# Optimization experiments

Measured on AMD Instinct MI355X. Metric: run time of the kernel, lower is better.

Reference implementation:

```python
import jax, jax.numpy as jnp
import numpy as np

EPS = 1e-5
S = 192  # seq_len = 24*8
D = 512
DFF = 2048


def setup_inputs() -> dict:
    key = jax.random.key(0)
    ks = jax.random.split(key, 8)
    tgt = jax.random.normal(ks[0], (64, 24, 8, D), jnp.float32)
    memory = jax.random.normal(ks[1], (64, 24, 8, D), jnp.float32)
    W1 = jax.random.normal(ks[2], (D, D), jnp.float32) * 0.02
    b1 = jnp.zeros((D,), jnp.float32)
    se = jax.random.normal(ks[3], (S, S), jnp.float32)
    score_embed = (se + se.T).reshape(1, 1, S, S)
    W2 = jax.random.normal(ks[4], (DFF, S), jnp.float32) * 0.05
    b2 = jnp.zeros((DFF,), jnp.float32)
    W3 = jax.random.normal(ks[5], (1, DFF), jnp.float32) * 0.02
    b3 = jnp.zeros((1,), jnp.float32)
    return {
        'tgt': tgt, 'memory': memory,
        'W1': W1, 'b1': b1, 'score_embed': score_embed,
        'g1': jnp.ones((1,), jnp.float32), 'be1': jnp.zeros((1,), jnp.float32),
        'W2': W2, 'b2': b2,
        'g2': jnp.ones((DFF,), jnp.float32), 'be2': jnp.zeros((DFF,), jnp.float32),
        'W3': W3, 'b3': b3,
        'g3': jnp.ones((1,), jnp.float32), 'be3': jnp.zeros((1,), jnp.float32),
    }


def _bn(x, gamma, beta, axes):
    # BatchNorm in training mode: biased variance over `axes`.
    mean = jnp.mean(x, axis=axes, keepdims=True)
    var = jnp.mean((x - mean) ** 2, axis=axes, keepdims=True)
    return gamma * (x - mean) * jax.lax.rsqrt(var + EPS) + beta


def reference(tgt, memory, W1, b1, score_embed, g1, be1, W2, b2, g2, be2, W3, b3, g3, be3):
    q = tgt.shape[0]
    k = memory.shape[0]
    d = tgt.shape[-1]
    tgt = tgt.reshape(q, S, d)      # [q, t, d]
    memory = memory.reshape(k, S, d)  # [k, s, d]
    query = tgt @ W1.T + b1
    key = memory @ W1.T + b1
    # bilinear score with learned symmetric bias: [q, k, s, t]
    score = jnp.einsum('qtd,ksd->qkst', query, key) * jax.nn.sigmoid(score_embed)
    score = score.reshape(q * k, S, S)
    # dual-axis max pooling, concat -> [q*k, 2S]
    score = jnp.concatenate((score.max(axis=1), score.max(axis=2)), axis=-1)
    x = score.reshape(-1, 1, S)                       # [2qk, 1, S]
    x = _bn(x, g1.reshape(1, 1, 1), be1.reshape(1, 1, 1), (0, 2)).reshape(-1, S)
    x = x @ W2.T + b2                                 # [2qk, DFF]
    x = _bn(x, g2, be2, (0,))
    x = jax.nn.relu(x)
    x = x @ W3.T + b3                                 # [2qk, 1]
    x = x.reshape(-1, 2).sum(axis=-1, keepdims=True)  # [qk, 1]
    x = _bn(x, g3, be3, (0,))
    return x.reshape(q, k)
```

## Files before the change

### kernel.cpp

```cpp
#include <hip/hip_runtime.h>

#define SS 192
#define DD 512
#define DFF 2048
#define NROW 12288
#define EPSV 1e-5f

using bf16x8 = __attribute__((ext_vector_type(8))) __bf16;
using f32x4  = __attribute__((ext_vector_type(4))) float;

__device__ inline unsigned short f2bf(float f) {
    unsigned u = __float_as_uint(f);
    unsigned r = (u + 0x7FFFu + ((u >> 16) & 1u)) >> 16;
    return (unsigned short)r;
}
__device__ inline float bf2f(unsigned short h) {
    return __uint_as_float(((unsigned)h) << 16);
}
__device__ inline unsigned f2mono(float f) {
    unsigned u = __float_as_uint(f);
    return u ^ ((unsigned)((int)u >> 31) | 0x80000000u);
}
__device__ inline float mono2f(unsigned u) {
    unsigned b = (u & 0x80000000u) ? (u ^ 0x80000000u) : ~u;
    return __uint_as_float(b);
}
#define ENC_NEGINF 0x007FFFFFu

#define GLL16(g, l) __builtin_amdgcn_global_load_lds( \
    (const __attribute__((address_space(1))) void*)(g), \
    (__attribute__((address_space(3))) void*)(l), 16, 0, 0)

template<int NW>
__device__ inline float blockReduceSum(float v) {
    __shared__ float red[NW];
    #pragma unroll
    for (int o = 32; o > 0; o >>= 1) v += __shfl_down(v, o);
    int w = threadIdx.x >> 6;
    __syncthreads();
    if ((threadIdx.x & 63) == 0) red[w] = v;
    __syncthreads();
    if (threadIdx.x == 0) {
        float t = 0;
        #pragma unroll
        for (int i = 0; i < NW; i++) t += red[i];
        red[0] = t;
    }
    __syncthreads();
    return red[0];
}

__global__ void k_cvt(const float* __restrict__ src, unsigned short* __restrict__ dst) {
    int i = blockIdx.x * 256 + threadIdx.x;
    float4 v = ((const float4*)src)[i];
    unsigned short o[4] = { f2bf(v.x), f2bf(v.y), f2bf(v.z), f2bf(v.w) };
    ((uint2*)dst)[i] = *(uint2*)o;
}

__global__ void k_sig(const float* __restrict__ se, float* __restrict__ sig) {
    int i = blockIdx.x * 256 + threadIdx.x;
    sig[i] = 1.0f / (1.0f + __expf(-se[i]));
}

__global__ void k_rowsum(const float* __restrict__ W2, float* __restrict__ rowsum) {
    int f = blockIdx.x * 256 + threadIdx.x;
    float s = 0.f;
    for (int i = 0; i < SS; i++) s += W2[(size_t)f * SS + i];
    rowsum[f] = s;
}

__global__ __launch_bounds__(256) void k_proj(
    const unsigned short* __restrict__ xbf, const unsigned short* __restrict__ w1bf,
    const float* __restrict__ b1, unsigned short* __restrict__ outQK)
{
    __shared__ unsigned short sA[3][128 * 32];
    __shared__ unsigned short sB[3][128 * 32];
    const int tid = threadIdx.x;
    const int lane = tid & 63;
    const int w = tid >> 6;
    const int m0 = blockIdx.x * 128;
    const int n0 = blockIdx.y * 128;
    const int wm = (w >> 1) * 64, wn = (w & 1) * 64;

    f32x4 acc[4][4] = {};

    const int sr  = lane >> 2;
    const int scg = (lane & 3) ^ ((lane >> 3) & 3);
    const unsigned short* Ab = xbf  + (size_t)m0 * DD;
    const unsigned short* Bb = w1bf + (size_t)n0 * DD;
    const unsigned short* AsrcB = Ab + (size_t)(w * 2 * 16 + sr) * DD + scg * 8;
    const unsigned short* BsrcB = Bb + (size_t)(w * 2 * 16 + sr) * DD + scg * 8;

    const int l16 = lane & 15, g = lane >> 4;
    const int cswz = ((g ^ ((l16 >> 1) & 3))) * 8;

    #pragma unroll
    for (int pt = 0; pt < 2; pt++) {
        #pragma unroll
        for (int i = 0; i < 2; i++) {
            int rb = w * 2 + i;
            GLL16(AsrcB + (size_t)i * 16 * DD + pt * 32, &sA[pt][rb * 512]);
            GLL16(BsrcB + (size_t)i * 16 * DD + pt * 32, &sB[pt][rb * 512]);
        }
    }

    #pragma unroll
    for (int t = 0; t < 16; t++) {
        if (t < 15) asm volatile("s_waitcnt vmcnt(4)" ::: "memory");
        else        asm volatile("s_waitcnt vmcnt(0)" ::: "memory");
        __builtin_amdgcn_s_barrier();
        if (t + 2 < 16) {
            const int buf = (t + 2) % 3;
            const int k0  = (t + 2) * 32;
            #pragma unroll
            for (int i = 0; i < 2; i++) {
                int rb = w * 2 + i;
                GLL16(AsrcB + (size_t)i * 16 * DD + k0, &sA[buf][rb * 512]);
                GLL16(BsrcB + (size_t)i * 16 * DD + k0, &sB[buf][rb * 512]);
            }
        }
        const int cur = t % 3;
        const unsigned short* aBase = &sA[cur][(wm + l16) * 32 + cswz];
        const unsigned short* bBase = &sB[cur][(wn + l16) * 32 + cswz];
        bf16x8 af[4];
        #pragma unroll
        for (int mi = 0; mi < 4; mi++) af[mi] = *(const bf16x8*)(aBase + mi * 512);
        __builtin_amdgcn_s_setprio(1);
        #pragma unroll
        for (int ni = 0; ni < 4; ni++) {
            bf16x8 bfr = *(const bf16x8*)(bBase + ni * 512);
            #pragma unroll
            for (int mi = 0; mi < 4; mi++)
                acc[mi][ni] = __builtin_amdgcn_mfma_f32_16x16x32_bf16(af[mi], bfr, acc[mi][ni], 0, 0, 0);
        }
        __builtin_amdgcn_s_setprio(0);
    }

    const int rg = lane >> 4;
    #pragma unroll
    for (int ni = 0; ni < 4; ni++) {
        int e = n0 + wn + ni * 16 + l16;
        float bias = b1[e];
        #pragma unroll
        for (int mi = 0; mi < 4; mi++) {
            #pragma unroll
            for (int r = 0; r < 4; r++) {
                int row = m0 + wm + mi * 16 + rg * 4 + r;
                outQK[(size_t)row * DD + e] = f2bf(acc[mi][ni][r] + bias);
            }
        }
    }
}

__global__ __launch_bounds__(1024, 4) void k_score(
    const unsigned short* __restrict__ qB,
    const unsigned short* __restrict__ kB,
    const float* __restrict__ sig,
    float* __restrict__ pooled)
{
    __shared__ unsigned short sA[3][192 * 32];
    __shared__ unsigned short sB[3][192 * 32];
    __shared__ unsigned maxT[192];
    __shared__ unsigned maxS[192];

    const int tid = threadIdx.x;
    const int p = blockIdx.x;
    const int q = p >> 6, kk = p & 63;
    const unsigned short* Ab = kB + (size_t)kk * SS * DD;
    const unsigned short* Bb = qB + (size_t)q * SS * DD;

    if (tid < 192) { maxT[tid] = ENC_NEGINF; maxS[tid] = ENC_NEGINF; }

    const int lane = tid & 63, w = tid >> 6;
    const int wsr = (w >> 2) * 48;
    const int wtc = (w & 3) * 48;

    f32x4 acc[3][3] = {};

    const int sr  = lane >> 2;
    const int scg = (lane & 3) ^ ((lane >> 3) & 3);
    const bool stager = (w < 12);
    const bool isA = (w < 6);
    const int wg = (isA ? w : (w - 6)) * 2;
    const unsigned short* srcB = (isA ? Ab : Bb) + (size_t)(wg * 16 + sr) * DD + scg * 8;
    unsigned short* dst0 = isA ? &sA[0][0] : &sB[0][0];

    const int l16 = lane & 15, g = lane >> 4;
    const int cswz = ((g ^ ((l16 >> 1) & 3))) * 8;

    if (stager) {
        #pragma unroll
        for (int pt = 0; pt < 2; pt++) {
            #pragma unroll
            for (int i = 0; i < 2; i++)
                GLL16(srcB + (size_t)i * 16 * DD + pt * 32, dst0 + pt * (192 * 32) + (wg + i) * 512);
        }
    }

    #pragma unroll
    for (int t = 0; t < 16; t++) {
        if (t < 15) asm volatile("s_waitcnt vmcnt(2)" ::: "memory");
        else        asm volatile("s_waitcnt vmcnt(0)" ::: "memory");
        __builtin_amdgcn_s_barrier();
        if (t + 2 < 16 && stager) {
            const int buf = (t + 2) % 3;
            const int k0  = (t + 2) * 32;
            #pragma unroll
            for (int i = 0; i < 2; i++)
                GLL16(srcB + (size_t)i * 16 * DD + k0, dst0 + buf * (192 * 32) + (wg + i) * 512);
        }
        const int cur = t % 3;
        const unsigned short* aBase = &sA[cur][(wsr + l16) * 32 + cswz];
        const unsigned short* bBase = &sB[cur][(wtc + l16) * 32 + cswz];
        bf16x8 af[3];
        #pragma unroll
        for (int mi = 0; mi < 3; mi++) af[mi] = *(const bf16x8*)(aBase + mi * 512);
        __builtin_amdgcn_s_setprio(1);
        #pragma unroll
        for (int ni = 0; ni < 3; ni++) {
            bf16x8 bfr = *(const bf16x8*)(bBase + ni * 512);
            #pragma unroll
            for (int mi = 0; mi < 3; mi++)
                acc[mi][ni] = __builtin_amdgcn_mfma_f32_16x16x32_bf16(af[mi], bfr, acc[mi][ni], 0, 0, 0);
        }
        __builtin_amdgcn_s_setprio(0);
    }

    const int rg = lane >> 4;

    #pragma unroll
    for (int mi = 0; mi < 3; mi++) {
        #pragma unroll
        for (int r = 0; r < 4; r++) {
            int s = wsr + mi * 16 + rg * 4 + r;
            const float* srow = sig + (size_t)s * SS + wtc;
            #pragma unroll
            for (int ni = 0; ni < 3; ni++)
                acc[mi][ni][r] *= srow[ni * 16 + l16];
        }
    }

    #pragma unroll
    for (int ni = 0; ni < 3; ni++) {
        float cm = -INFINITY;
        #pragma unroll
        for (int mi = 0; mi < 3; mi++)
            #pragma unroll
            for (int r = 0; r < 4; r++)
                cm = fmaxf(cm, acc[mi][ni][r]);
        cm = fmaxf(cm, __shfl_xor(cm, 16));
        cm = fmaxf(cm, __shfl_xor(cm, 32));
        if (lane < 16) atomicMax(&maxT[wtc + ni * 16 + lane], f2mono(cm));
    }
    #pragma unroll
    for (int mi = 0; mi < 3; mi++) {
        #pragma unroll
        for (int r = 0; r < 4; r++) {
            float rm = -INFINITY;
            #pragma unroll
            for (int ni = 0; ni < 3; ni++) rm = fmaxf(rm, acc[mi][ni][r]);
            rm = fmaxf(rm, __shfl_xor(rm, 1));
            rm = fmaxf(rm, __shfl_xor(rm, 2));
            rm = fmaxf(rm, __shfl_xor(rm, 4));
            rm = fmaxf(rm, __shfl_xor(rm, 8));
            if ((lane & 15) == 0)
                atomicMax(&maxS[wsr + mi * 16 + rg * 4 + r], f2mono(rm));
        }
    }
    __syncthreads();
    float* out = pooled + (size_t)p * 384;
    if (tid < 192) {
        out[tid]       = mono2f(maxT[tid]);
        out[192 + tid] = mono2f(maxS[tid]);
    }
}

__global__ __launch_bounds__(256) void k_bn1(const float* __restrict__ pooled, float* __restrict__ bn1) {
    float s = 0.f, ss = 0.f;
    size_t base = (size_t)blockIdx.x * 8192;
    for (int i = 0; i < 32; i++) {
        float v = pooled[base + i * 256 + threadIdx.x];
        s += v; ss += v * v;
    }
    s  = blockReduceSum<4>(s);
    ss = blockReduceSum<4>(ss);
    if (threadIdx.x == 0) { atomicAdd(&bn1[0], s); atomicAdd(&bn1[1], ss); }
}

__global__ __launch_bounds__(256) void k_w2(
    const float* __restrict__ x, const float* __restrict__ W2,
    const float* __restrict__ b2, const float* __restrict__ rowsum,
    const float* __restrict__ bn1, const float* __restrict__ g1,
    const float* __restrict__ be1, unsigned short* __restrict__ z,
    float* __restrict__ cs, float* __restrict__ css)
{
    __shared__ unsigned short lA[128][40];
    __shared__ unsigned short lB[128][40];
    const int tid = threadIdx.x;
    const int lane = tid & 63;
    const int w = tid >> 6;
    const int m0 = blockIdx.x * 128;
    const int n0 = blockIdx.y * 128;
    const int wm = (w >> 1) * 64, wn = (w & 1) * 64;

    f32x4 acc[4][4] = {};
    const int srow = tid >> 1;
    const int scol = (tid & 1) * 16;
    const float* Asrc = x  + (size_t)(m0 + srow) * SS;
    const float* Bsrc = W2 + (size_t)(n0 + srow) * SS;

    for (int k0 = 0; k0 < SS; k0 += 32) {
        {
            unsigned short tmp[16];
            const float4* s4 = (const float4*)(Asrc + k0 + scol);
            #pragma unroll
            for (int i = 0; i < 4; i++) {
                float4 v = s4[i];
                tmp[i*4+0] = f2bf(v.x); tmp[i*4+1] = f2bf(v.y);
                tmp[i*4+2] = f2bf(v.z); tmp[i*4+3] = f2bf(v.w);
            }
            *(uint4*)(&lA[srow][scol])     = *(uint4*)(&tmp[0]);
            *(uint4*)(&lA[srow][scol + 8]) = *(uint4*)(&tmp[8]);
            const float4* t4 = (const float4*)(Bsrc + k0 + scol);
            #pragma unroll
            for (int i = 0; i < 4; i++) {
                float4 v = t4[i];
                tmp[i*4+0] = f2bf(v.x); tmp[i*4+1] = f2bf(v.y);
                tmp[i*4+2] = f2bf(v.z); tmp[i*4+3] = f2bf(v.w);
            }
            *(uint4*)(&lB[srow][scol])     = *(uint4*)(&tmp[0]);
            *(uint4*)(&lB[srow][scol + 8]) = *(uint4*)(&tmp[8]);
        }
        __syncthreads();
        const int l16 = lane & 15, kg = (lane >> 4) * 8;
        bf16x8 af[4];
        #pragma unroll
        for (int mi = 0; mi < 4; mi++)
            af[mi] = *(const bf16x8*)(&lA[wm + mi*16 + l16][kg]);
        #pragma unroll
        for (int ni = 0; ni < 4; ni++) {
            bf16x8 bfr = *(const bf16x8*)(&lB[wn + ni*16 + l16][kg]);
            #pragma unroll
            for (int mi = 0; mi < 4; mi++)
                acc[mi][ni] = __builtin_amdgcn_mfma_f32_16x16x32_bf16(af[mi], bfr, acc[mi][ni], 0, 0, 0);
        }
        __syncthreads();
    }

    const float n1 = 8192.0f * 192.0f;
    const float m1 = bn1[0] / n1;
    const float v1 = bn1[1] / n1 - m1 * m1;
    const float a1 = g1[0] * rsqrtf(v1 + EPSV);
    const float c1 = be1[0] - m1 * a1;

    float* colsum = (float*)&lA[0][0];
    float* colssq = colsum + 128;
    if (tid < 128) { colsum[tid] = 0.f; colssq[tid] = 0.f; }
    __syncthreads();

    const int l16 = lane & 15, rg = lane >> 4;
    #pragma unroll
    for (int ni = 0; ni < 4; ni++) {
        int lc = wn + ni*16 + l16;
        int f = n0 + lc;
        float add = c1 * rowsum[f] + b2[f];
        float s_ = 0.f, ss_ = 0.f;
        #pragma unroll
        for (int mi = 0; mi < 4; mi++) {
            #pragma unroll
            for (int r = 0; r < 4; r++) {
                int row = m0 + wm + mi*16 + rg*4 + r;
                float y = a1 * acc[mi][ni][r] + add;
                z[(size_t)row * DFF + f] = f2bf(y);
                s_ += y; ss_ += y * y;
            }
        }
        atomicAdd(&colsum[lc], s_);
        atomicAdd(&colssq[lc], ss_);
    }
    __syncthreads();
    if (tid < 128) {
        atomicAdd(&cs[n0 + tid],  colsum[tid]);
        atomicAdd(&css[n0 + tid], colssq[tid]);
    }
}

__global__ __launch_bounds__(256) void k_final_dot(
    const unsigned short* __restrict__ z, const float* __restrict__ cs,
    const float* __restrict__ css, const float* __restrict__ g2,
    const float* __restrict__ be2, const float* __restrict__ W3,
    const float* __restrict__ b3, float* __restrict__ rowout)
{
    const int lane = threadIdx.x & 63, w = threadIdx.x >> 6;
    float4 av[4][2], cv[4][2], wv[4][2];
    #pragma unroll
    for (int c = 0; c < 4; c++) {
        int col = c * 512 + lane * 8;
        #pragma unroll
        for (int h = 0; h < 2; h++) {
            float4 csv  = *(const float4*)(cs  + col + 4*h);
            float4 cssv = *(const float4*)(css + col + 4*h);
            float4 g2v  = *(const float4*)(g2  + col + 4*h);
            float4 be2v = *(const float4*)(be2 + col + 4*h);
            wv[c][h]    = *(const float4*)(W3  + col + 4*h);
            float* mp = (float*)&csv; float* sp = (float*)&cssv;
            float* gp = (float*)&g2v; float* bp = (float*)&be2v;
            float* ap = (float*)&av[c][h]; float* cp = (float*)&cv[c][h];
            #pragma unroll
            for (int j = 0; j < 4; j++) {
                float m  = mp[j] * (1.0f / 8192.0f);
                float vr = sp[j] * (1.0f / 8192.0f) - m * m;
                float a  = gp[j] * rsqrtf(vr + EPSV);
                ap[j] = a;
                cp[j] = bp[j] - m * a;
            }
        }
    }
    const float bias = b3[0];
    int r0 = blockIdx.x * 16 + w * 4;
    #pragma unroll
    for (int rr = 0; rr < 4; rr++) {
        int row = r0 + rr;
        float sum = 0.f;
        #pragma unroll
        for (int c = 0; c < 4; c++) {
            uint4 v = *(const uint4*)(z + (size_t)row * DFF + c * 512 + lane * 8);
            unsigned short pv[8];
            *(uint4*)pv = v;
            #pragma unroll
            for (int j = 0; j < 8; j++) {
                float a = ((const float*)&av[c][j >> 2])[j & 3];
                float cc = ((const float*)&cv[c][j >> 2])[j & 3];
                float wf = ((const float*)&wv[c][j >> 2])[j & 3];
                float x = a * bf2f(pv[j]) + cc;
                sum += fmaxf(x, 0.f) * wf;
            }
        }
        #pragma unroll
        for (int o = 32; o > 0; o >>= 1) sum += __shfl_down(sum, o);
        if (lane == 0) rowout[row] = sum + bias;
    }
}

__global__ __launch_bounds__(1024) void k_out(
    const float* __restrict__ rowout, const float* __restrict__ g3,
    const float* __restrict__ be3, float* __restrict__ out)
{
    float pv0, pv1, pv2, pv3;
    float s = 0.f, ss = 0.f;
    {
        int p0 = threadIdx.x;
        pv0 = rowout[2*p0] + rowout[2*p0+1];
        int p1 = 1024 + threadIdx.x;
        pv1 = rowout[2*p1] + rowout[2*p1+1];
        int p2 = 2048 + threadIdx.x;
        pv2 = rowout[2*p2] + rowout[2*p2+1];
        int p3 = 3072 + threadIdx.x;
        pv3 = rowout[2*p3] + rowout[2*p3+1];
        s = pv0 + pv1 + pv2 + pv3;
        ss = pv0*pv0 + pv1*pv1 + pv2*pv2 + pv3*pv3;
    }
    s  = blockReduceSum<16>(s);
    ss = blockReduceSum<16>(ss);
    float m  = s * (1.0f / 4096.0f);
    float vr = ss * (1.0f / 4096.0f) - m * m;
    float a  = g3[0] * rsqrtf(vr + EPSV);
    float c  = be3[0] - m * a;
    out[threadIdx.x]        = a * pv0 + c;
    out[1024 + threadIdx.x] = a * pv1 + c;
    out[2048 + threadIdx.x] = a * pv2 + c;
    out[3072 + threadIdx.x] = a * pv3 + c;
}

extern "C" void kernel_launch(void* const* d_in, const int* in_sizes, int n_in,
                              void* d_out, int out_size, void* d_ws, size_t ws_size,
                              hipStream_t stream)
{
    const float* tgt = (const float*)d_in[0];
    const float* mem = (const float*)d_in[1];
    const float* W1  = (const float*)d_in[2];
    const float* b1  = (const float*)d_in[3];
    const float* se  = (const float*)d_in[4];
    const float* g1  = (const float*)d_in[5];
    const float* be1 = (const float*)d_in[6];
    const float* W2  = (const float*)d_in[7];
    const float* b2  = (const float*)d_in[8];
    const float* g2  = (const float*)d_in[9];
    const float* be2 = (const float*)d_in[10];
    const float* W3  = (const float*)d_in[11];
    const float* b3  = (const float*)d_in[12];
    const float* g3  = (const float*)d_in[13];
    const float* be3 = (const float*)d_in[14];
    float* out = (float*)d_out;

    char* ws = (char*)d_ws;
    size_t off = 0;
    auto alloc = [&](size_t bytes) { void* p = ws + off; off += (bytes + 255) & ~(size_t)255; return p; };

    char* region0 = (char*)alloc((size_t)8192 * DFF * 2);
    unsigned short* xbf = (unsigned short*)region0;
    unsigned short* z   = (unsigned short*)region0;
    unsigned short* qk  = (unsigned short*)alloc((size_t)24576 * DD * 2);
    unsigned short* w1bf= (unsigned short*)alloc((size_t)DD * DD * 2);
    float* sig          = (float*)alloc((size_t)SS * SS * 4);
    float* pooled       = (float*)alloc((size_t)4096 * 384 * 4);
    float* rowsum       = (float*)alloc(DFF * 4);
    float* stats        = (float*)alloc((2 + 2 * DFF) * 4);
    float* rowout       = (float*)alloc(8192 * 4);

    float* bn1 = stats;
    float* cs  = stats + 2;
    float* css = stats + 2 + DFF;

    hipMemsetAsync(stats, 0, (2 + 2 * DFF) * 4, stream);

    k_cvt<<<6144, 256, 0, stream>>>(tgt, xbf);
    k_cvt<<<6144, 256, 0, stream>>>(mem, xbf + (size_t)NROW * DD);
    k_cvt<<<256,  256, 0, stream>>>(W1, w1bf);
    k_sig<<<144, 256, 0, stream>>>(se, sig);
    k_rowsum<<<8, 256, 0, stream>>>(W2, rowsum);
    k_proj<<<dim3(192, 4), 256, 0, stream>>>(xbf, w1bf, b1, qk);
    k_score<<<4096, 1024, 0, stream>>>(qk, qk + (size_t)NROW * DD, sig, pooled);
    k_bn1<<<192, 256, 0, stream>>>(pooled, bn1);
    k_w2<<<dim3(64, 16), 256, 0, stream>>>(pooled, W2, b2, rowsum, bn1, g1, be1, z, cs, css);
    k_final_dot<<<512, 256, 0, stream>>>(z, cs, css, g2, be2, W3, b3, rowout);
    k_out<<<1, 1024, 0, stream>>>(rowout, g3, be3, out);
}
```

Baseline: 329.4 us.

## Pre-convert W2 and pooled to bf16 and pipeline k_w2 with async LDS loads

Merges the small preprocessing kernels into two launches: one converts tgt and memory to bf16, one builds W1 bf16, the sigmoid table, rowsum and a new bf16 copy of W2. k_bn1 now also writes a bf16 copy of the pooled scores. k_w2 drops its per-tile fp32 load and convert and instead uses triple-buffered, swizzled direct global-to-LDS loads with a waitcnt and barrier pipeline, the same scheme as k_proj. This adds an extra buffer write in bn1 and more launch-side work in exchange for a leaner GEMM main loop with fewer launches.

After: 313.3 us, median of 2. 4.9% less time.

```diff
diff --git a/kernel.cpp b/kernel.cpp
--- a/kernel.cpp
+++ b/kernel.cpp
@@ -50,23 +50,41 @@
     return red[0];
 }
 
-__global__ void k_cvt(const float* __restrict__ src, unsigned short* __restrict__ dst) {
+__global__ void k_cvt2(const float* __restrict__ a, const float* __restrict__ b,
+                       unsigned short* __restrict__ dst) {
     int i = blockIdx.x * 256 + threadIdx.x;
-    float4 v = ((const float4*)src)[i];
+    const int half = NROW * DD / 4;
+    const float* src = (i < half) ? a : b;
+    int j = (i < half) ? i : i - half;
+    float4 v = ((const float4*)src)[j];
     unsigned short o[4] = { f2bf(v.x), f2bf(v.y), f2bf(v.z), f2bf(v.w) };
     ((uint2*)dst)[i] = *(uint2*)o;
 }
 
-__global__ void k_sig(const float* __restrict__ se, float* __restrict__ sig) {
-    int i = blockIdx.x * 256 + threadIdx.x;
-    sig[i] = 1.0f / (1.0f + __expf(-se[i]));
-}
-
-__global__ void k_rowsum(const float* __restrict__ W2, float* __restrict__ rowsum) {
-    int f = blockIdx.x * 256 + threadIdx.x;
-    float s = 0.f;
-    for (int i = 0; i < SS; i++) s += W2[(size_t)f * SS + i];
-    rowsum[f] = s;
+__global__ void k_prep(const float* __restrict__ W1, const float* __restrict__ se,
+                       const float* __restrict__ W2,
+                       unsigned short* __restrict__ w1bf, float* __restrict__ sig,
+                       float* __restrict__ rowsum, unsigned short* __restrict__ w2bf) {
+    int bid = blockIdx.x;
+    if (bid < 256) {
+        int i = bid * 256 + threadIdx.x;
+        float4 v = ((const float4*)W1)[i];
+        unsigned short o[4] = { f2bf(v.x), f2bf(v.y), f2bf(v.z), f2bf(v.w) };
+        ((uint2*)w1bf)[i] = *(uint2*)o;
+    } else if (bid < 400) {
+        int i = (bid - 256) * 256 + threadIdx.x;
+        sig[i] = 1.0f / (1.0f + __expf(-se[i]));
+    } else if (bid < 408) {
+        int f = (bid - 400) * 256 + threadIdx.x;
+        float s = 0.f;
+        for (int i = 0; i < SS; i++) s += W2[(size_t)f * SS + i];
+        rowsum[f] = s;
+    } else {
+        int i = (bid - 408) * 256 + threadIdx.x;
+        float4 v = ((const float4*)W2)[i];
+        unsigned short o[4] = { f2bf(v.x), f2bf(v.y), f2bf(v.z), f2bf(v.w) };
+        ((uint2*)w2bf)[i] = *(uint2*)o;
+    }
 }
 
 __global__ __launch_bounds__(256) void k_proj(
@@ -275,12 +293,16 @@
     }
 }
 
-__global__ __launch_bounds__(256) void k_bn1(const float* __restrict__ pooled, float* __restrict__ bn1) {
+__global__ __launch_bounds__(256) void k_bn1(const float* __restrict__ pooled,
+                                             float* __restrict__ bn1,
+                                             unsigned short* __restrict__ pooledbf) {
     float s = 0.f, ss = 0.f;
     size_t base = (size_t)blockIdx.x * 8192;
     for (int i = 0; i < 32; i++) {
-        float v = pooled[base + i * 256 + threadIdx.x];
+        size_t idx = base + i * 256 + threadIdx.x;
+        float v = pooled[idx];
         s += v; ss += v * v;
+        pooledbf[idx] = f2bf(v);
     }
     s  = blockReduceSum<4>(s);
     ss = blockReduceSum<4>(ss);
@@ -288,14 +310,14 @@
 }
 
 __global__ __launch_bounds__(256) void k_w2(
-    const float* __restrict__ x, const float* __restrict__ W2,
+    const unsigned short* __restrict__ xbf, const unsigned short* __restrict__ w2bf,
     const float* __restrict__ b2, const float* __restrict__ rowsum,
     const float* __restrict__ bn1, const float* __restrict__ g1,
     const float* __restrict__ be1, unsigned short* __restrict__ z,
     float* __restrict__ cs, float* __restrict__ css)
 {
-    __shared__ unsigned short lA[128][40];
-    __shared__ unsigned short lB[128][40];
+    __shared__ unsigned short sA[3][128 * 32];
+    __shared__ unsigned short sB[3][128 * 32];
     const int tid = threadIdx.x;
     const int lane = tid & 63;
     const int w = tid >> 6;
@@ -304,47 +326,55 @@
     const int wm = (w >> 1) * 64, wn = (w & 1) * 64;
 
     f32x4 acc[4][4] = {};
-    const int srow = tid >> 1;
-    const int scol = (tid & 1) * 16;
-    const float* Asrc = x  + (size_t)(m0 + srow) * SS;
-    const float* Bsrc = W2 + (size_t)(n0 + srow) * SS;
-
-    for (int k0 = 0; k0 < SS; k0 += 32) {
-        {
-            unsigned short tmp[16];
-            const float4* s4 = (const float4*)(Asrc + k0 + scol);
-            #pragma unroll
-            for (int i = 0; i < 4; i++) {
-                float4 v = s4[i];
-                tmp[i*4+0] = f2bf(v.x); tmp[i*4+1] = f2bf(v.y);
-                tmp[i*4+2] = f2bf(v.z); tmp[i*4+3] = f2bf(v.w);
+
+    const int sr  = lane >> 2;
+    const int scg = (lane & 3) ^ ((lane >> 3) & 3);
+    const unsigned short* AsrcB = xbf  + (size_t)(m0 + w * 32 + sr) * SS + scg * 8;
+    const unsigned short* BsrcB = w2bf + (size_t)(n0 + w * 32 + sr) * SS + scg * 8;
+
+    const int l16 = lane & 15, g = lane >> 4;
+    const int cswz = ((g ^ ((l16 >> 1) & 3))) * 8;
+
+    #pragma unroll
+    for (int pt = 0; pt < 2; pt++) {
+        #pragma unroll
+        for (int i = 0; i < 2; i++) {
+            int rb = w * 2 + i;
+            GLL16(AsrcB + (size_t)i * 16 * SS + pt * 32, &sA[pt][rb * 512]);
+            GLL16(BsrcB + (size_t)i * 16 * SS + pt * 32, &sB[pt][rb * 512]);
+        }
+    }
+
+    #pragma unroll
+    for (int t = 0; t < 6; t++) {
+        if (t < 5) asm volatile("s_waitcnt vmcnt(4)" ::: "memory");
+        else       asm volatile("s_waitcnt vmcnt(0)" ::: "memory");
+        __builtin_amdgcn_s_barrier();
+        if (t + 2 < 6) {
+            const int buf = (t + 2) % 3;
+            const int k0  = (t + 2) * 32;
+            #pragma unroll
+            for (int i = 0; i < 2; i++) {
+                int rb = w * 2 + i;
+                GLL16(AsrcB + (size_t)i * 16 * SS + k0, &sA[buf][rb * 512]);
+                GLL16(BsrcB + (size_t)i * 16 * SS + k0, &sB[buf][rb * 512]);
             }
-            *(uint4*)(&lA[srow][scol])     = *(uint4*)(&tmp[0]);
-            *(uint4*)(&lA[srow][scol + 8]) = *(uint4*)(&tmp[8]);
-            const float4* t4 = (const float4*)(Bsrc + k0 + scol);
-            #pragma unroll
-            for (int i = 0; i < 4; i++) {
-                float4 v = t4[i];
-                tmp[i*4+0] = f2bf(v.x); tmp[i*4+1] = f2bf(v.y);
-                tmp[i*4+2] = f2bf(v.z); tmp[i*4+3] = f2bf(v.w);
-            }
-            *(uint4*)(&lB[srow][scol])     = *(uint4*)(&tmp[0]);
-            *(uint4*)(&lB[srow][scol + 8]) = *(uint4*)(&tmp[8]);
-        }
-        __syncthreads();
-        const int l16 = lane & 15, kg = (lane >> 4) * 8;
+        }
+        const int cur = t % 3;
+        const unsigned short* aBase = &sA[cur][(wm + l16) * 32 + cswz];
+        const unsigned short* bBase = &sB[cur][(wn + l16) * 32 + cswz];
         bf16x8 af[4];
         #pragma unroll
-        for (int mi = 0; mi < 4; mi++)
-            af[mi] = *(const bf16x8*)(&lA[wm + mi*16 + l16][kg]);
+        for (int mi = 0; mi < 4; mi++) af[mi] = *(const bf16x8*)(aBase + mi * 512);
+        __builtin_amdgcn_s_setprio(1);
         #pragma unroll
         for (int ni = 0; ni < 4; ni++) {
-            bf16x8 bfr = *(const bf16x8*)(&lB[wn + ni*16 + l16][kg]);
+            bf16x8 bfr = *(const bf16x8*)(bBase + ni * 512);
             #pragma unroll
             for (int mi = 0; mi < 4; mi++)
                 acc[mi][ni] = __builtin_amdgcn_mfma_f32_16x16x32_bf16(af[mi], bfr, acc[mi][ni], 0, 0, 0);
         }
-        __syncthreads();
+        __builtin_amdgcn_s_setprio(0);
     }
 
     const float n1 = 8192.0f * 192.0f;
@@ -353,15 +383,16 @@
     const float a1 = g1[0] * rsqrtf(v1 + EPSV);
     const float c1 = be1[0] - m1 * a1;
 
-    float* colsum = (float*)&lA[0][0];
+    float* colsum = (float*)&sA[0][0];
     float* colssq = colsum + 128;
+    __syncthreads();
     if (tid < 128) { colsum[tid] = 0.f; colssq[tid] = 0.f; }
     __syncthreads();
 
-    const int l16 = lane & 15, rg = lane >> 4;
+    const int rg = lane >> 4;
     #pragma unroll
     for (int ni = 0; ni < 4; ni++) {
-        int lc = wn + ni*16 + l16;
+        int lc = wn + ni * 16 + l16;
         int f = n0 + lc;
         float add = c1 * rowsum[f] + b2[f];
         float s_ = 0.f, ss_ = 0.f;
@@ -369,7 +400,7 @@
         for (int mi = 0; mi < 4; mi++) {
             #pragma unroll
             for (int r = 0; r < 4; r++) {
-                int row = m0 + wm + mi*16 + rg*4 + r;
+                int row = m0 + wm + mi * 16 + rg * 4 + r;
                 float y = a1 * acc[mi][ni][r] + add;
                 z[(size_t)row * DFF + f] = f2bf(y);
                 s_ += y; ss_ += y * y;
@@ -502,8 +533,10 @@
     unsigned short* z   = (unsigned short*)region0;
     unsigned short* qk  = (unsigned short*)alloc((size_t)24576 * DD * 2);
     unsigned short* w1bf= (unsigned short*)alloc((size_t)DD * DD * 2);
+    unsigned short* w2bf= (unsigned short*)alloc((size_t)DFF * SS * 2);
     float* sig          = (float*)alloc((size_t)SS * SS * 4);
     float* pooled       = (float*)alloc((size_t)4096 * 384 * 4);
+    unsigned short* pooledbf = (unsigned short*)alloc((size_t)4096 * 384 * 2);
     float* rowsum       = (float*)alloc(DFF * 4);
     float* stats        = (float*)alloc((2 + 2 * DFF) * 4);
     float* rowout       = (float*)alloc(8192 * 4);
@@ -514,15 +547,12 @@
 
     hipMemsetAsync(stats, 0, (2 + 2 * DFF) * 4, stream);
 
-    k_cvt<<<6144, 256, 0, stream>>>(tgt, xbf);
-    k_cvt<<<6144, 256, 0, stream>>>(mem, xbf + (size_t)NROW * DD);
-    k_cvt<<<256,  256, 0, stream>>>(W1, w1bf);
-    k_sig<<<144, 256, 0, stream>>>(se, sig);
-    k_rowsum<<<8, 256, 0, stream>>>(W2, rowsum);
+    k_cvt2<<<12288, 256, 0, stream>>>(tgt, mem, xbf);
+    k_prep<<<792, 256, 0, stream>>>(W1, se, W2, w1bf, sig, rowsum, w2bf);
     k_proj<<<dim3(192, 4), 256, 0, stream>>>(xbf, w1bf, b1, qk);
     k_score<<<4096, 1024, 0, stream>>>(qk, qk + (size_t)NROW * DD, sig, pooled);
-    k_bn1<<<192, 256, 0, stream>>>(pooled, bn1);
-    k_w2<<<dim3(64, 16), 256, 0, stream>>>(pooled, W2, b2, rowsum, bn1, g1, be1, z, cs, css);
+    k_bn1<<<192, 256, 0, stream>>>(pooled, bn1, pooledbf);
+    k_w2<<<dim3(64, 16), 256, 0, stream>>>(pooledbf, w2bf, b2, rowsum, bn1, g1, be1, z, cs, css);
     k_final_dot<<<512, 256, 0, stream>>>(z, cs, css, g2, be2, W3, b3, rowout);
     k_out<<<1, 1024, 0, stream>>>(rowout, g3, be3, out);
 }
```
